# Kernel optimization log

Measured on AMD Instinct MI355X. Metric: run time of the kernel, lower is better.

The kernel has to match this reference:

```python
import jax, jax.numpy as jnp
import numpy as np

HID = 128
HEADS = 4
CH = HID // HEADS          # 32
EDGE_DIM = 2 * HID         # H_update mode
GROUPS = 8
NEG_SLOPE = 0.2
EPS_GN = 1e-5
EPS_LN = 1e-5
N_NODES = 32768
N_EDGES = 524288


def setup_inputs() -> dict:
    key = jax.random.key(0)
    ks = jax.random.split(key, 32)
    N, E, C = N_NODES, N_EDGES, HID
    s = lambda fan: 1.0 / np.sqrt(fan)
    inp = dict(
        h_target=jax.random.normal(ks[0], (N, C), jnp.float32),
        h_source=jax.random.normal(ks[1], (N, C), jnp.float32),
        pos=jax.random.normal(ks[2], (N, 2), jnp.float32),
        t_emb=jax.random.normal(ks[3], (N, C), jnp.float32),
        edge_index=jax.random.randint(ks[4], (2, E), 0, N, jnp.int32),
        # AdaGN params
        gn_gamma=jnp.ones((C,), jnp.float32),
        gn_beta=jnp.zeros((C,), jnp.float32),
        fc_W=jax.random.normal(ks[5], (C, 2 * C), jnp.float32) * s(C),
        fc_b=jnp.zeros((2 * C,), jnp.float32),
        # GATv2 params
        Wl=jax.random.normal(ks[6], (C, HEADS * CH), jnp.float32) * s(C),
        bl=jnp.zeros((HEADS * CH,), jnp.float32),
        Wr=jax.random.normal(ks[7], (C, HEADS * CH), jnp.float32) * s(C),
        br=jnp.zeros((HEADS * CH,), jnp.float32),
        We=jax.random.normal(ks[8], (EDGE_DIM, HEADS * CH), jnp.float32) * s(EDGE_DIM),
        att=jax.random.normal(ks[9], (HEADS, CH), jnp.float32) * s(CH),
        gat_bias=jnp.zeros((HEADS * CH,), jnp.float32),
        # post GAT linear
        Wpost=jax.random.normal(ks[10], (C, C), jnp.float32) * s(C),
        bpost=jnp.zeros((C,), jnp.float32),
        # update MLP: LayerNorm -> Linear -> GELU -> Linear
        ln_g=jnp.ones((C,), jnp.float32),
        ln_b=jnp.zeros((C,), jnp.float32),
        W1=jax.random.normal(ks[11], (C, C), jnp.float32) * s(C),
        b1=jnp.zeros((C,), jnp.float32),
        W2=jax.random.normal(ks[12], (C, C), jnp.float32) * s(C),
        b2=jnp.zeros((C,), jnp.float32),
    )
    return inp


def _adagn(x, cond, gn_gamma, gn_beta, fc_W, fc_b):
    N, C = x.shape
    xg = x.reshape(N, GROUPS, C // GROUPS)
    mu = xg.mean(-1, keepdims=True)
    var = xg.var(-1, keepdims=True)
    normed = ((xg - mu) * jax.lax.rsqrt(var + EPS_GN)).reshape(N, C)
    normed = normed * gn_gamma + gn_beta
    style = cond @ fc_W + fc_b
    gamma, beta = jnp.split(style, 2, axis=-1)
    return normed * (1.0 + gamma) + beta


def reference(h_target, h_source, pos, t_emb, edge_index,
              gn_gamma, gn_beta, fc_W, fc_b,
              Wl, bl, Wr, br, We, att, gat_bias,
              Wpost, bpost, ln_g, ln_b, W1, b1, W2, b2):
    N, C = h_source.shape
    src, dst = edge_index[0], edge_index[1]

    h_src_mod = _adagn(h_source, t_emb, gn_gamma, gn_beta, fc_W, fc_b)

    # physics edge features (H_update mode)
    d_vec = pos[src] - pos[dst]                       # [E,2]
    dx, dy = d_vec[:, 0:1], d_vec[:, 1:2]
    dist_sq = jnp.maximum((d_vec ** 2).sum(-1, keepdims=True), 1e-8)
    grad_mag = (h_src_mod[src] - h_src_mod[dst]) / dist_sq   # [E,C]
    edge_attr = jnp.concatenate([grad_mag * (-dy), grad_mag * dx], axis=-1)  # [E,2C]

    # GATv2Conv (eval mode, no dropout)
    xl = (h_src_mod @ Wl + bl).reshape(N, HEADS, CH)  # source transform
    xr = (h_src_mod @ Wr + br).reshape(N, HEADS, CH)  # target transform
    e = (edge_attr @ We).reshape(-1, HEADS, CH)
    z = jax.nn.leaky_relu(xl[src] + xr[dst] + e, NEG_SLOPE)   # [E,H,Ch]
    logit = jnp.einsum('ehc,hc->eh', z, att)                  # [E,H]
    m = jax.ops.segment_max(logit, dst, num_segments=N)       # [N,H]
    m = jnp.where(jnp.isfinite(m), m, 0.0)
    ex = jnp.exp(logit - m[dst])
    denom = jax.ops.segment_sum(ex, dst, num_segments=N)      # [N,H]
    alpha = ex / (denom[dst] + 1e-16)                         # [E,H]
    msg = xl[src] * alpha[..., None]                          # [E,H,Ch]
    aggr = jax.ops.segment_sum(msg, dst, num_segments=N).reshape(N, HEADS * CH)
    aggr = aggr + gat_bias

    aggr = aggr @ Wpost + bpost

    # update MLP with residual
    mu = aggr.mean(-1, keepdims=True)
    var = aggr.var(-1, keepdims=True)
    ln = (aggr - mu) * jax.lax.rsqrt(var + EPS_LN) * ln_g + ln_b
    h = jax.nn.gelu(ln @ W1 + b1, approximate=False) @ W2 + b2
    return h_target + h
```

## Files before the change

kernel.cpp:

```cpp
#include <hip/hip_runtime.h>
#include <hip/hip_bf16.h>
#include <math.h>

#define HID 128

typedef __bf16 bf16x8 __attribute__((ext_vector_type(8)));
typedef float f32x4 __attribute__((ext_vector_type(4)));
typedef float nf4 __attribute__((ext_vector_type(4)));
union BF8 { uint4 u; bf16x8 v; unsigned short s[8]; };

__device__ __forceinline__ unsigned short f2bf(float x) {
  unsigned u = __float_as_uint(x);
  unsigned r = u + 0x7FFFu + ((u >> 16) & 1u);
  return (unsigned short)(r >> 16);
}
__device__ __forceinline__ float bf2f(unsigned short h) {
  return __uint_as_float(((unsigned)h) << 16);
}
__device__ __forceinline__ void ld2bf(const unsigned short* p, float& x, float& y) {
  unsigned v = *(const unsigned*)p;
  x = __uint_as_float((v & 0xFFFFu) << 16);
  y = __uint_as_float(v & 0xFFFF0000u);
}
__device__ __forceinline__ float2 pk_add2(float2 a, float2 b) {
  return make_float2(a.x + b.x, a.y + b.y);
}
__device__ __forceinline__ float2 pk_sub2(float2 a, float2 b) {
  return make_float2(a.x - b.x, a.y - b.y);
}
__device__ __forceinline__ float2 pk_fma2(float2 a, float2 b, float2 c) {
  return make_float2(fmaf(a.x, b.x, c.x), fmaf(a.y, b.y, c.y));
}
__device__ __forceinline__ float2 pk_max2(float2 a, float2 b) {
  return make_float2(fmaxf(a.x, b.x), fmaxf(a.y, b.y));
}
__device__ __forceinline__ float2 pk_muls2(float2 a, float b) {
  return make_float2(a.x * b, a.y * b);
}

__global__ void prep3(const float* __restrict__ fc_W, const float* __restrict__ Wl,
                      const float* __restrict__ Wr, const float* __restrict__ We,
                      const float* __restrict__ Wpost, const float* __restrict__ W1,
                      const float* __restrict__ W2, const float* __restrict__ bl,
                      const float* __restrict__ br, const float* __restrict__ gat_bias,
                      const float* __restrict__ bpost,
                      unsigned short* __restrict__ fcTh, unsigned short* __restrict__ fcTl,
                      unsigned short* __restrict__ WnTh, unsigned short* __restrict__ WnTl,
                      unsigned short* __restrict__ WpT, unsigned short* __restrict__ W1T,
                      unsigned short* __restrict__ W2T,
                      float* __restrict__ bxy, float* __restrict__ bpost2) {
  int gid = blockIdx.x * 256 + threadIdx.x;
  if (gid < 32768) {
    int n = gid >> 7, k = gid & 127;
    float x = fc_W[k * 256 + n];
    unsigned short h = f2bf(x);
    fcTh[n * 128 + k] = h;
    fcTl[n * 128 + k] = f2bf(x - bf2f(h));
  } else if (gid < 98304) {
    int i = gid - 32768; int n = i >> 7, k = i & 127;
    float x;
    if (n < 128)      x = Wl[k * 128 + n];
    else if (n < 256) x = Wr[k * 128 + (n - 128)];
    else if (n < 384) x = We[k * 128 + (n - 256)];
    else              x = We[(128 + k) * 128 + (n - 384)];
    unsigned short h = f2bf(x);
    WnTh[n * 128 + k] = h;
    if (n >= 256) WnTl[(n - 256) * 128 + k] = f2bf(x - bf2f(h));
  } else if (gid < 147456) {
    int i = gid - 98304; int which = i >> 14; int j = i & 16383;
    int n = j >> 7, k = j & 127;
    const float* W = (which == 0) ? Wpost : (which == 1) ? W1 : W2;
    unsigned short* T = (which == 0) ? WpT : (which == 1) ? W1T : W2T;
    T[n * 128 + k] = f2bf(W[k * 128 + n]);
  } else if (gid < 147712) {
    int j = gid - 147456;
    bxy[j] = (j < 128) ? bl[j] : br[j - 128];
  } else if (gid < 147840) {
    int t = gid - 147712;
    float s = bpost[t];
    for (int k = 0; k < 128; ++k) s += gat_bias[k] * Wpost[k * 128 + t];
    bpost2[t] = s;
  }
}

__global__ __launch_bounds__(256) void gemm_mfma(const float* __restrict__ A,
                                                 const unsigned short* __restrict__ WTh,
                                                 const unsigned short* __restrict__ WTl,
                                                 const float* __restrict__ bias,
                                                 float* __restrict__ C, int Ncols) {
  int tid = threadIdx.x;
  int wave = tid >> 6, lane = tid & 63;
  int m = lane & 15, q = lane >> 4;
  int r0 = blockIdx.x * 64 + wave * 16;
  const float* arow = A + (size_t)(r0 + m) * 128 + q * 8;
  BF8 Ah[4], Al[4];
#pragma unroll
  for (int kc = 0; kc < 4; ++kc) {
    float4 x0 = *(const float4*)(arow + kc * 32);
    float4 x1 = *(const float4*)(arow + kc * 32 + 4);
    float xs[8] = {x0.x, x0.y, x0.z, x0.w, x1.x, x1.y, x1.z, x1.w};
#pragma unroll
    for (int j = 0; j < 8; ++j) {
      unsigned short h = f2bf(xs[j]);
      Ah[kc].s[j] = h;
      Al[kc].s[j] = f2bf(xs[j] - bf2f(h));
    }
  }
  int ntiles = Ncols >> 4;
  for (int nt = 0; nt < ntiles; ++nt) {
    const unsigned short* wr  = WTh + (size_t)(nt * 16 + m) * 128 + q * 8;
    const unsigned short* wrl = WTl + (size_t)(nt * 16 + m) * 128 + q * 8;
    f32x4 acc = {0.f, 0.f, 0.f, 0.f};
#pragma unroll
    for (int kc = 0; kc < 4; ++kc) {
      BF8 bh, blo;
      bh.u  = *(const uint4*)(wr + kc * 32);
      blo.u = *(const uint4*)(wrl + kc * 32);
      acc = __builtin_amdgcn_mfma_f32_16x16x32_bf16(Ah[kc].v, bh.v, acc, 0, 0, 0);
      acc = __builtin_amdgcn_mfma_f32_16x16x32_bf16(Al[kc].v, bh.v, acc, 0, 0, 0);
      acc = __builtin_amdgcn_mfma_f32_16x16x32_bf16(Ah[kc].v, blo.v, acc, 0, 0, 0);
    }
    int n = nt * 16 + m;
    float bv = bias ? bias[n] : 0.0f;
#pragma unroll
    for (int i = 0; i < 4; ++i) {
      int row = r0 + q * 4 + i;
      C[(size_t)row * Ncols + n] = acc[i] + bv;
    }
  }
}

__global__ __launch_bounds__(256) void k_nodeP(const float* __restrict__ h_source,
                                               const float* __restrict__ style,
                                               const float* __restrict__ gn_gamma,
                                               const float* __restrict__ gn_beta,
                                               const unsigned short* __restrict__ WnTh,
                                               const unsigned short* __restrict__ WnTl,
                                               const float* __restrict__ bxy,
                                               unsigned short* __restrict__ packed,
                                               unsigned short* __restrict__ xrArr) {
  int tid = threadIdx.x, wave = tid >> 6, lane = tid & 63;
  int m = lane & 15, q = lane >> 4;
  int r0 = blockIdx.x * 128 + wave * 32;
  BF8 Ah[2][4], Al[2][4];
#pragma unroll
  for (int set = 0; set < 2; ++set) {
    int r = r0 + set * 16 + m;
    const float* hrow = h_source + (size_t)r * 128;
    const float* srow = style + (size_t)r * 256;
#pragma unroll
    for (int kc = 0; kc < 4; ++kc) {
      int ch = q * 8 + kc * 32;
      float4 x0 = *(const float4*)(hrow + ch);
      float4 x1 = *(const float4*)(hrow + ch + 4);
      float xs[8] = {x0.x, x0.y, x0.z, x0.w, x1.x, x1.y, x1.z, x1.w};
      float s8 = 0.f, q8 = 0.f;
#pragma unroll
      for (int j = 0; j < 8; ++j) { s8 += xs[j]; q8 += xs[j] * xs[j]; }
      float s16 = s8 + __shfl_xor(s8, 16);
      float q16 = q8 + __shfl_xor(q8, 16);
      float mu = s16 * (1.0f / 16.0f);
      float var = q16 * (1.0f / 16.0f) - mu * mu;
      float rv = rsqrtf(var + 1e-5f);
      float4 g0 = *(const float4*)(gn_gamma + ch);
      float4 g1 = *(const float4*)(gn_gamma + ch + 4);
      float4 be0 = *(const float4*)(gn_beta + ch);
      float4 be1 = *(const float4*)(gn_beta + ch + 4);
      float4 sg0 = *(const float4*)(srow + ch);
      float4 sg1 = *(const float4*)(srow + ch + 4);
      float4 sb0 = *(const float4*)(srow + 128 + ch);
      float4 sb1 = *(const float4*)(srow + 128 + ch + 4);
      float gg[8] = {g0.x, g0.y, g0.z, g0.w, g1.x, g1.y, g1.z, g1.w};
      float bb[8] = {be0.x, be0.y, be0.z, be0.w, be1.x, be1.y, be1.z, be1.w};
      float sg[8] = {sg0.x, sg0.y, sg0.z, sg0.w, sg1.x, sg1.y, sg1.z, sg1.w};
      float sb[8] = {sb0.x, sb0.y, sb0.z, sb0.w, sb1.x, sb1.y, sb1.z, sb1.w};
#pragma unroll
      for (int j = 0; j < 8; ++j) {
        float v = ((xs[j] - mu) * rv * gg[j] + bb[j]) * (1.0f + sg[j]) + sb[j];
        unsigned short h = f2bf(v);
        Ah[set][kc].s[j] = h;
        Al[set][kc].s[j] = f2bf(v - bf2f(h));
      }
    }
  }
  for (int nt = 0; nt < 32; ++nt) {
    f32x4 acc0 = {0.f, 0.f, 0.f, 0.f};
    f32x4 acc1 = {0.f, 0.f, 0.f, 0.f};
    const unsigned short* wr = WnTh + (size_t)(nt * 16 + m) * 128 + q * 8;
    if (nt < 16) {
#pragma unroll
      for (int kc = 0; kc < 4; ++kc) {
        BF8 bh; bh.u = *(const uint4*)(wr + kc * 32);
        acc0 = __builtin_amdgcn_mfma_f32_16x16x32_bf16(Ah[0][kc].v, bh.v, acc0, 0, 0, 0);
        acc1 = __builtin_amdgcn_mfma_f32_16x16x32_bf16(Ah[1][kc].v, bh.v, acc1, 0, 0, 0);
      }
    } else {
      const unsigned short* wl = WnTl + (size_t)((nt - 16) * 16 + m) * 128 + q * 8;
#pragma unroll
      for (int kc = 0; kc < 4; ++kc) {
        BF8 bh, blo;
        bh.u  = *(const uint4*)(wr + kc * 32);
        blo.u = *(const uint4*)(wl + kc * 32);
        acc0 = __builtin_amdgcn_mfma_f32_16x16x32_bf16(Ah[0][kc].v, bh.v, acc0, 0, 0, 0);
        acc0 = __builtin_amdgcn_mfma_f32_16x16x32_bf16(Al[0][kc].v, bh.v, acc0, 0, 0, 0);
        acc0 = __builtin_amdgcn_mfma_f32_16x16x32_bf16(Ah[0][kc].v, blo.v, acc0, 0, 0, 0);
        acc1 = __builtin_amdgcn_mfma_f32_16x16x32_bf16(Ah[1][kc].v, bh.v, acc1, 0, 0, 0);
        acc1 = __builtin_amdgcn_mfma_f32_16x16x32_bf16(Al[1][kc].v, bh.v, acc1, 0, 0, 0);
        acc1 = __builtin_amdgcn_mfma_f32_16x16x32_bf16(Ah[1][kc].v, blo.v, acc1, 0, 0, 0);
      }
    }
    int n = nt * 16 + m;
    float bv = (nt < 16) ? bxy[n] : 0.0f;
#pragma unroll
    for (int set = 0; set < 2; ++set) {
      f32x4 a = set ? acc1 : acc0;
#pragma unroll
      for (int i = 0; i < 4; ++i) {
        int row = r0 + set * 16 + q * 4 + i;
        unsigned short h = f2bf(a[i] + bv);
        if (nt < 8)       packed[(size_t)row * 384 + n] = h;
        else if (nt < 16) xrArr[(size_t)row * 128 + (n - 128)] = h;
        else              packed[(size_t)row * 384 + 128 + (n - 256)] = h;
      }
    }
  }
}

__global__ __launch_bounds__(256) void k_hist(const int* __restrict__ edst,
                                              int* __restrict__ count, int E) {
  int e = blockIdx.x * 256 + threadIdx.x;
  if (e < E) atomicAdd(&count[edst[e]], 1);
}

__global__ __launch_bounds__(1024) void k_scan(const int* __restrict__ count,
                                               int* __restrict__ rowptr,
                                               int* __restrict__ cursor, int N, int E) {
  __shared__ int wtot[16];
  int t = threadIdx.x;
  int lane = t & 63, wv = t >> 6;
  int base4 = t * 8;
  int4 L[8];
  int s = 0;
#pragma unroll
  for (int i = 0; i < 8; ++i) {
    L[i] = ((const int4*)count)[base4 + i];
    s += L[i].x + L[i].y + L[i].z + L[i].w;
  }
  int incl = s;
#pragma unroll
  for (int off = 1; off < 64; off <<= 1) {
    int v = __shfl_up(incl, off);
    if (lane >= off) incl += v;
  }
  if (lane == 63) wtot[wv] = incl;
  __syncthreads();
  if (t < 16) {
    int v = wtot[t];
    int sc = v;
#pragma unroll
    for (int off = 1; off < 16; off <<= 1) {
      int u = __shfl_up(sc, off, 16);
      if (t >= off) sc += u;
    }
    wtot[t] = sc - v;
  }
  __syncthreads();
  int run = wtot[wv] + (incl - s);
#pragma unroll
  for (int i = 0; i < 8; ++i) {
    int4 c = L[i];
    int4 r;
    r.x = run; run += c.x;
    r.y = run; run += c.y;
    r.z = run; run += c.z;
    r.w = run; run += c.w;
    ((int4*)rowptr)[base4 + i] = r;
    ((int4*)cursor)[base4 + i] = r;
  }
  if (t == 1023) rowptr[N] = E;
}

__global__ __launch_bounds__(256) void k_scatter(const int* __restrict__ esrc,
                                                 const int* __restrict__ edst,
                                                 const float* __restrict__ pos,
                                                 int* __restrict__ cursor,
                                                 nf4* __restrict__ meta, int E) {
  int e = blockIdx.x * 256 + threadIdx.x;
  if (e >= E) return;
  int src = esrc[e], dst = edst[e];
  int p = atomicAdd(&cursor[dst], 1);
  float2 ps = *(const float2*)(pos + 2 * src);
  float2 pd = *(const float2*)(pos + 2 * dst);
  float dx = ps.x - pd.x, dy = ps.y - pd.y;
  float d2 = fmaxf(dx * dx + dy * dy, 1e-8f);
  nf4 v = {__int_as_float(src), -dy / d2, dx / d2, 0.0f};
  __builtin_nontemporal_store(v, &meta[p]);
}

__device__ __forceinline__ void edge_step(nf4 mt, const unsigned* __restrict__ packedW,
                                          int lane, float2 xr, float2 Ad, float2 Bd,
                                          float a0, float a1,
                                          float& m, float& l, float2& s) {
  int si = __float_as_int(mt.x);
  const unsigned* pr = packedW + (size_t)si * 192;
  unsigned wxl = pr[lane];
  unsigned wA  = pr[64 + lane];
  unsigned wB  = pr[128 + lane];
  float2 xl = make_float2(__uint_as_float(wxl << 16), __uint_as_float(wxl & 0xFFFF0000u));
  float2 A  = make_float2(__uint_as_float(wA << 16),  __uint_as_float(wA & 0xFFFF0000u));
  float2 B  = make_float2(__uint_as_float(wB << 16),  __uint_as_float(wB & 0xFFFF0000u));
  float2 z = pk_add2(xl, xr);
  z = pk_fma2(make_float2(mt.y, mt.y), pk_sub2(A, Ad), z);
  z = pk_fma2(make_float2(mt.z, mt.z), pk_sub2(B, Bd), z);
  float2 zl = pk_max2(z, pk_muls2(z, 0.2f));
  float p = fmaf(a0, zl.x, a1 * zl.y);
#pragma unroll
  for (int mm = 8; mm >= 1; mm >>= 1) p += __shfl_xor(p, mm);
  if (p <= m) {
    float ex = expf(p - m);
    l += ex;
    s = pk_fma2(make_float2(ex, ex), xl, s);
  } else {
    float sc = expf(m - p);
    l = fmaf(l, sc, 1.0f);
    s = pk_fma2(make_float2(sc, sc), s, xl);
    m = p;
  }
}

__global__ __launch_bounds__(256) void k_edge(const int* __restrict__ rowptr,
                                              const nf4* __restrict__ meta,
                                              const unsigned short* __restrict__ packed,
                                              const unsigned short* __restrict__ xrArr,
                                              const float* __restrict__ att,
                                              float* __restrict__ aggr, int N) {
  int tid = threadIdx.x;
  int d = blockIdx.x * 4 + (tid >> 6);
  if (d >= N) return;
  int lane = tid & 63;
  int c0 = lane * 2;
  float2 av = *(const float2*)(att + c0);
  const unsigned* packedW = (const unsigned*)packed;
  float2 xr, Ad, Bd;
  ld2bf(xrArr + (size_t)d * 128 + c0, xr.x, xr.y);
  {
    const unsigned* pd = packedW + (size_t)d * 192;
    unsigned wA = pd[64 + lane], wB = pd[128 + lane];
    Ad = make_float2(__uint_as_float(wA << 16), __uint_as_float(wA & 0xFFFF0000u));
    Bd = make_float2(__uint_as_float(wB << 16), __uint_as_float(wB & 0xFFFF0000u));
  }
  int beg = rowptr[d], end = rowptr[d + 1];
  float m1 = -INFINITY, l1 = 0.f; float2 s1 = make_float2(0.f, 0.f);
  float m2 = -INFINITY, l2 = 0.f; float2 s2 = make_float2(0.f, 0.f);
  int j = beg;
  for (; j + 1 < end; j += 2) {
    nf4 mta = __builtin_nontemporal_load(&meta[j]);
    nf4 mtb = __builtin_nontemporal_load(&meta[j + 1]);
    edge_step(mta, packedW, lane, xr, Ad, Bd, av.x, av.y, m1, l1, s1);
    edge_step(mtb, packedW, lane, xr, Ad, Bd, av.x, av.y, m2, l2, s2);
  }
  if (j < end) {
    nf4 mta = __builtin_nontemporal_load(&meta[j]);
    edge_step(mta, packedW, lane, xr, Ad, Bd, av.x, av.y, m1, l1, s1);
  }
  float nm = fmaxf(m1, m2);
  float sc1 = (m1 == nm) ? 1.0f : expf(m1 - nm);
  float sc2 = (m2 == nm) ? 1.0f : expf(m2 - nm);
  float l = fmaf(l1, sc1, l2 * sc2);
  float o0 = fmaf(s1.x, sc1, s2.x * sc2);
  float o1 = fmaf(s1.y, sc1, s2.y * sc2);
  float inv = 1.0f / (l + 1e-16f);
  *(float2*)&aggr[(size_t)d * 128 + c0] = make_float2(o0 * inv, o1 * inv);
}

__global__ __launch_bounds__(256) void k_mlp(const float* __restrict__ aggr,
                                             const unsigned short* __restrict__ WpT,
                                             const unsigned short* __restrict__ W1T,
                                             const unsigned short* __restrict__ W2T,
                                             const float* __restrict__ bpost2,
                                             const float* __restrict__ b1,
                                             const float* __restrict__ b2,
                                             const float* __restrict__ ln_g,
                                             const float* __restrict__ ln_b,
                                             const float* __restrict__ h_target,
                                             float* __restrict__ out) {
  __shared__ unsigned short Tb[64 * 136];
  __shared__ unsigned short Ub[64 * 136];
  int tid = threadIdx.x, wave = tid >> 6, lane = tid & 63;
  int m = lane & 15, q = lane >> 4;
  int r0 = blockIdx.x * 64 + wave * 16;
  int rb0 = wave * 16;
  BF8 Af[4];
  {
    const float* arow = aggr + (size_t)(r0 + m) * 128 + q * 8;
#pragma unroll
    for (int kc = 0; kc < 4; ++kc) {
      float4 x0 = *(const float4*)(arow + kc * 32);
      float4 x1 = *(const float4*)(arow + kc * 32 + 4);
      float xs[8] = {x0.x, x0.y, x0.z, x0.w, x1.x, x1.y, x1.z, x1.w};
#pragma unroll
      for (int jj = 0; jj < 8; ++jj) Af[kc].s[jj] = f2bf(xs[jj]);
    }
  }
  f32x4 acc[8];
#pragma unroll
  for (int t = 0; t < 8; ++t) {
    const unsigned short* wr = WpT + (size_t)(t * 16 + m) * 128 + q * 8;
    f32x4 a = {0.f, 0.f, 0.f, 0.f};
#pragma unroll
    for (int kc = 0; kc < 4; ++kc) {
      BF8 bh; bh.u = *(const uint4*)(wr + kc * 32);
      a = __builtin_amdgcn_mfma_f32_16x16x32_bf16(Af[kc].v, bh.v, a, 0, 0, 0);
    }
    acc[t] = a;
  }
  float sum[4] = {0, 0, 0, 0}, sq[4] = {0, 0, 0, 0};
#pragma unroll
  for (int t = 0; t < 8; ++t) {
    float bv = bpost2[t * 16 + m];
#pragma unroll
    for (int i = 0; i < 4; ++i) {
      float v = acc[t][i] + bv;
      acc[t][i] = v;
      sum[i] += v;
      sq[i] += v * v;
    }
  }
#pragma unroll
  for (int i = 0; i < 4; ++i) {
#pragma unroll
    for (int w = 1; w <= 8; w <<= 1) {
      sum[i] += __shfl_xor(sum[i], w);
      sq[i] += __shfl_xor(sq[i], w);
    }
  }
  float mu[4], rv[4];
#pragma unroll
  for (int i = 0; i < 4; ++i) {
    mu[i] = sum[i] * (1.0f / 128.0f);
    float var = sq[i] * (1.0f / 128.0f) - mu[i] * mu[i];
    rv[i] = rsqrtf(var + 1e-5f);
  }
#pragma unroll
  for (int t = 0; t < 8; ++t) {
    int n = t * 16 + m;
    float g = ln_g[n], b = ln_b[n];
#pragma unroll
    for (int i = 0; i < 4; ++i) {
      float v = (acc[t][i] - mu[i]) * rv[i] * g + b;
      Tb[(rb0 + q * 4 + i) * 136 + n] = f2bf(v);
    }
  }
  __syncthreads();
  BF8 Bf[4];
  {
    const unsigned short* tp = Tb + (rb0 + m) * 136 + q * 8;
#pragma unroll
    for (int kc = 0; kc < 4; ++kc) Bf[kc].u = *(const uint4*)(tp + kc * 32);
  }
#pragma unroll
  for (int t = 0; t < 8; ++t) {
    const unsigned short* wr = W1T + (size_t)(t * 16 + m) * 128 + q * 8;
    f32x4 a = {0.f, 0.f, 0.f, 0.f};
#pragma unroll
    for (int kc = 0; kc < 4; ++kc) {
      BF8 bh; bh.u = *(const uint4*)(wr + kc * 32);
      a = __builtin_amdgcn_mfma_f32_16x16x32_bf16(Bf[kc].v, bh.v, a, 0, 0, 0);
    }
    acc[t] = a;
  }
#pragma unroll
  for (int t = 0; t < 8; ++t) {
    int n = t * 16 + m;
    float bv = b1[n];
#pragma unroll
    for (int i = 0; i < 4; ++i) {
      float v = acc[t][i] + bv;
      v = 0.5f * v * (1.0f + erff(v * 0.70710678118654752f));
      Ub[(rb0 + q * 4 + i) * 136 + n] = f2bf(v);
    }
  }
  __syncthreads();
  BF8 Cf[4];
  {
    const unsigned short* up = Ub + (rb0 + m) * 136 + q * 8;
#pragma unroll
    for (int kc = 0; kc < 4; ++kc) Cf[kc].u = *(const uint4*)(up + kc * 32);
  }
#pragma unroll
  for (int t = 0; t < 8; ++t) {
    const unsigned short* wr = W2T + (size_t)(t * 16 + m) * 128 + q * 8;
    f32x4 a = {0.f, 0.f, 0.f, 0.f};
#pragma unroll
    for (int kc = 0; kc < 4; ++kc) {
      BF8 bh; bh.u = *(const uint4*)(wr + kc * 32);
      a = __builtin_amdgcn_mfma_f32_16x16x32_bf16(Cf[kc].v, bh.v, a, 0, 0, 0);
    }
    int n = t * 16 + m;
    float bv = b2[n];
#pragma unroll
    for (int i = 0; i < 4; ++i) {
      size_t off = (size_t)(r0 + q * 4 + i) * 128 + n;
      out[off] = a[i] + bv + h_target[off];
    }
  }
}

extern "C" void kernel_launch(void* const* d_in, const int* in_sizes, int n_in,
                              void* d_out, int out_size, void* d_ws, size_t ws_size,
                              hipStream_t stream) {
  const float* h_target = (const float*)d_in[0];
  const float* h_source = (const float*)d_in[1];
  const float* pos      = (const float*)d_in[2];
  const float* t_emb    = (const float*)d_in[3];
  const int*   eidx     = (const int*)d_in[4];
  const float* gn_gamma = (const float*)d_in[5];
  const float* gn_beta  = (const float*)d_in[6];
  const float* fc_W     = (const float*)d_in[7];
  const float* fc_b     = (const float*)d_in[8];
  const float* Wl       = (const float*)d_in[9];
  const float* bl       = (const float*)d_in[10];
  const float* Wr       = (const float*)d_in[11];
  const float* br       = (const float*)d_in[12];
  const float* We       = (const float*)d_in[13];
  const float* att      = (const float*)d_in[14];
  const float* gat_bias = (const float*)d_in[15];
  const float* Wpost    = (const float*)d_in[16];
  const float* bpost    = (const float*)d_in[17];
  const float* ln_g     = (const float*)d_in[18];
  const float* ln_b     = (const float*)d_in[19];
  const float* W1       = (const float*)d_in[20];
  const float* b1       = (const float*)d_in[21];
  const float* W2       = (const float*)d_in[22];
  const float* b2       = (const float*)d_in[23];

  const int N = in_sizes[0] / HID;
  const int E = in_sizes[4] / 2;
  const int* esrc = eidx;
  const int* edst = eidx + E;

  float* ws = (float*)d_ws;
  const size_t MF = 1024 * 1024;
  float* style  = ws;
  float* aggr   = ws;
  unsigned short* packed = (unsigned short*)(ws + 8 * MF);
  unsigned short* xrArr  = (unsigned short*)(ws + 14 * MF);
  nf4*   meta   = (nf4*)(ws + 16 * MF);
  int*   rowptr = (int*)(ws + 18 * MF);
  int*   count  = rowptr + 32832;
  int*   cursor = count + 32832;
  unsigned short* wgt = (unsigned short*)(ws + 18 * MF + 131072);
  unsigned short* fcTh = wgt;
  unsigned short* fcTl = wgt + 32768;
  unsigned short* WnTh = wgt + 65536;
  unsigned short* WnTl = wgt + 131072;
  unsigned short* WpT  = wgt + 163840;
  unsigned short* W1T  = wgt + 180224;
  unsigned short* W2T  = wgt + 196608;
  float* bxy    = (float*)(wgt + 212992);
  float* bpost2 = bxy + 256;
  const size_t needed = (size_t)(18 * MF + 131072 + 106496 + 512) * 4;
  if (ws_size < needed) return;

  dim3 blk(256);

  prep3<<<578, blk, 0, stream>>>(fc_W, Wl, Wr, We, Wpost, W1, W2, bl, br, gat_bias, bpost,
                                 fcTh, fcTl, WnTh, WnTl, WpT, W1T, W2T, bxy, bpost2);
  gemm_mfma<<<N / 64, blk, 0, stream>>>(t_emb, fcTh, fcTl, fc_b, style, 256);
  k_nodeP<<<N / 128, blk, 0, stream>>>(h_source, style, gn_gamma, gn_beta, WnTh, WnTl, bxy,
                                       packed, xrArr);
  (void)hipMemsetAsync(count, 0, (size_t)N * 4, stream);
  k_hist<<<(E + 255) / 256, blk, 0, stream>>>(edst, count, E);
  k_scan<<<1, 1024, 0, stream>>>(count, rowptr, cursor, N, E);
  k_scatter<<<(E + 255) / 256, blk, 0, stream>>>(esrc, edst, pos, cursor, meta, E);
  k_edge<<<(N + 3) / 4, blk, 0, stream>>>(rowptr, meta, packed, xrArr, att, aggr, N);
  k_mlp<<<N / 64, blk, 0, stream>>>(aggr, WpT, W1T, W2T, bpost2, b1, b2, ln_g, ln_b,
                                    h_target, (float*)d_out);
}
```

Measured before the change: 394.1 us.

## Fuse CSR build stages into node-side kernels to cut launches

The separate histogram, scan and scatter kernels are folded into the weight-prep, style-GEMM and node-projection kernels as extra block ranges, so independent work shares each launch and the launch count drops from eight to five. The scan is moved into a single 256-thread block inside the style GEMM kernel, where each thread serially sums 32 int4 values. The edge loop now software-prefetches the next pair of meta records and uses normal loads and stores instead of nontemporal ones. The scan block may lengthen the style kernel's tail, and the cache hint changes may alter memory behaviour.

```diff
diff --git a/kernel.cpp b/kernel.cpp
--- a/kernel.cpp
+++ b/kernel.cpp
@@ -38,18 +38,26 @@
   return make_float2(a.x * b, a.y * b);
 }
 
-__global__ void prep3(const float* __restrict__ fc_W, const float* __restrict__ Wl,
-                      const float* __restrict__ Wr, const float* __restrict__ We,
-                      const float* __restrict__ Wpost, const float* __restrict__ W1,
-                      const float* __restrict__ W2, const float* __restrict__ bl,
-                      const float* __restrict__ br, const float* __restrict__ gat_bias,
-                      const float* __restrict__ bpost,
-                      unsigned short* __restrict__ fcTh, unsigned short* __restrict__ fcTl,
-                      unsigned short* __restrict__ WnTh, unsigned short* __restrict__ WnTl,
-                      unsigned short* __restrict__ WpT, unsigned short* __restrict__ W1T,
-                      unsigned short* __restrict__ W2T,
-                      float* __restrict__ bxy, float* __restrict__ bpost2) {
-  int gid = blockIdx.x * 256 + threadIdx.x;
+__global__ __launch_bounds__(256) void k1_prep_hist(
+    const float* __restrict__ fc_W, const float* __restrict__ Wl,
+    const float* __restrict__ Wr, const float* __restrict__ We,
+    const float* __restrict__ Wpost, const float* __restrict__ W1,
+    const float* __restrict__ W2, const float* __restrict__ bl,
+    const float* __restrict__ br, const float* __restrict__ gat_bias,
+    const float* __restrict__ bpost,
+    unsigned short* __restrict__ fcTh, unsigned short* __restrict__ fcTl,
+    unsigned short* __restrict__ WnTh, unsigned short* __restrict__ WnTl,
+    unsigned short* __restrict__ WpT, unsigned short* __restrict__ W1T,
+    unsigned short* __restrict__ W2T,
+    float* __restrict__ bxy, float* __restrict__ bpost2,
+    const int* __restrict__ edst, int* __restrict__ count, int E) {
+  int bid = blockIdx.x;
+  if (bid >= 578) {
+    int e = (bid - 578) * 256 + threadIdx.x;
+    if (e < E) atomicAdd(&count[edst[e]], 1);
+    return;
+  }
+  int gid = bid * 256 + threadIdx.x;
   if (gid < 32768) {
     int n = gid >> 7, k = gid & 127;
     float x = fc_W[k * 256 + n];
@@ -83,11 +91,49 @@
   }
 }
 
-__global__ __launch_bounds__(256) void gemm_mfma(const float* __restrict__ A,
-                                                 const unsigned short* __restrict__ WTh,
-                                                 const unsigned short* __restrict__ WTl,
-                                                 const float* __restrict__ bias,
-                                                 float* __restrict__ C, int Ncols) {
+__global__ __launch_bounds__(256) void k2_style_scan(
+    const float* __restrict__ A, const unsigned short* __restrict__ WTh,
+    const unsigned short* __restrict__ WTl, const float* __restrict__ bias,
+    float* __restrict__ C,
+    const int* __restrict__ count, int* __restrict__ rowptr,
+    int* __restrict__ cursor, int N, int E) {
+  if (blockIdx.x == 512) {
+    __shared__ int wtot[4];
+    int t = threadIdx.x, lane = t & 63, wv = t >> 6;
+    const int4* c4 = (const int4*)count;
+    int base = t * 32;
+    int s = 0;
+    for (int i = 0; i < 32; ++i) {
+      int4 c = c4[base + i];
+      s += c.x + c.y + c.z + c.w;
+    }
+    int incl = s;
+#pragma unroll
+    for (int off = 1; off < 64; off <<= 1) {
+      int v = __shfl_up(incl, off);
+      if (lane >= off) incl += v;
+    }
+    if (lane == 63) wtot[wv] = incl;
+    __syncthreads();
+    if (t == 0) {
+      int a0 = wtot[0], a1 = wtot[1], a2 = wtot[2];
+      wtot[0] = 0; wtot[1] = a0; wtot[2] = a0 + a1; wtot[3] = a0 + a1 + a2;
+    }
+    __syncthreads();
+    int run = wtot[wv] + incl - s;
+    for (int i = 0; i < 32; ++i) {
+      int4 c = c4[base + i];
+      int4 r;
+      r.x = run; run += c.x;
+      r.y = run; run += c.y;
+      r.z = run; run += c.z;
+      r.w = run; run += c.w;
+      ((int4*)rowptr)[base + i] = r;
+      ((int4*)cursor)[base + i] = r;
+    }
+    if (t == 255) rowptr[N] = E;
+    return;
+  }
   int tid = threadIdx.x;
   int wave = tid >> 6, lane = tid & 63;
   int m = lane & 15, q = lane >> 4;
@@ -106,8 +152,7 @@
       Al[kc].s[j] = f2bf(xs[j] - bf2f(h));
     }
   }
-  int ntiles = Ncols >> 4;
-  for (int nt = 0; nt < ntiles; ++nt) {
+  for (int nt = 0; nt < 16; ++nt) {
     const unsigned short* wr  = WTh + (size_t)(nt * 16 + m) * 128 + q * 8;
     const unsigned short* wrl = WTl + (size_t)(nt * 16 + m) * 128 + q * 8;
     f32x4 acc = {0.f, 0.f, 0.f, 0.f};
@@ -121,27 +166,41 @@
       acc = __builtin_amdgcn_mfma_f32_16x16x32_bf16(Ah[kc].v, blo.v, acc, 0, 0, 0);
     }
     int n = nt * 16 + m;
-    float bv = bias ? bias[n] : 0.0f;
+    float bv = bias[n];
 #pragma unroll
     for (int i = 0; i < 4; ++i) {
       int row = r0 + q * 4 + i;
-      C[(size_t)row * Ncols + n] = acc[i] + bv;
-    }
-  }
-}
-
-__global__ __launch_bounds__(256) void k_nodeP(const float* __restrict__ h_source,
-                                               const float* __restrict__ style,
-                                               const float* __restrict__ gn_gamma,
-                                               const float* __restrict__ gn_beta,
-                                               const unsigned short* __restrict__ WnTh,
-                                               const unsigned short* __restrict__ WnTl,
-                                               const float* __restrict__ bxy,
-                                               unsigned short* __restrict__ packed,
-                                               unsigned short* __restrict__ xrArr) {
+      C[(size_t)row * 256 + n] = acc[i] + bv;
+    }
+  }
+}
+
+__global__ __launch_bounds__(256) void k3_node_scatter(
+    const float* __restrict__ h_source, const float* __restrict__ style,
+    const float* __restrict__ gn_gamma, const float* __restrict__ gn_beta,
+    const unsigned short* __restrict__ WnTh, const unsigned short* __restrict__ WnTl,
+    const float* __restrict__ bxy,
+    unsigned short* __restrict__ packed, unsigned short* __restrict__ xrArr,
+    const int* __restrict__ esrc, const int* __restrict__ edst,
+    const float* __restrict__ pos, int* __restrict__ cursor,
+    nf4* __restrict__ meta, int E) {
+  int bid = blockIdx.x;
+  if (bid >= 256) {
+    int e = (bid - 256) * 256 + threadIdx.x;
+    if (e >= E) return;
+    int src = esrc[e], dst = edst[e];
+    int p = atomicAdd(&cursor[dst], 1);
+    float2 ps = *(const float2*)(pos + 2 * src);
+    float2 pd = *(const float2*)(pos + 2 * dst);
+    float dx = ps.x - pd.x, dy = ps.y - pd.y;
+    float d2 = fmaxf(dx * dx + dy * dy, 1e-8f);
+    nf4 v = {__int_as_float(src), -dy / d2, dx / d2, 0.0f};
+    meta[p] = v;
+    return;
+  }
   int tid = threadIdx.x, wave = tid >> 6, lane = tid & 63;
   int m = lane & 15, q = lane >> 4;
-  int r0 = blockIdx.x * 128 + wave * 32;
+  int r0 = bid * 128 + wave * 32;
   BF8 Ah[2][4], Al[2][4];
 #pragma unroll
   for (int set = 0; set < 2; ++set) {
@@ -224,77 +283,6 @@
       }
     }
   }
-}
-
-__global__ __launch_bounds__(256) void k_hist(const int* __restrict__ edst,
-                                              int* __restrict__ count, int E) {
-  int e = blockIdx.x * 256 + threadIdx.x;
-  if (e < E) atomicAdd(&count[edst[e]], 1);
-}
-
-__global__ __launch_bounds__(1024) void k_scan(const int* __restrict__ count,
-                                               int* __restrict__ rowptr,
-                                               int* __restrict__ cursor, int N, int E) {
-  __shared__ int wtot[16];
-  int t = threadIdx.x;
-  int lane = t & 63, wv = t >> 6;
-  int base4 = t * 8;
-  int4 L[8];
-  int s = 0;
-#pragma unroll
-  for (int i = 0; i < 8; ++i) {
-    L[i] = ((const int4*)count)[base4 + i];
-    s += L[i].x + L[i].y + L[i].z + L[i].w;
-  }
-  int incl = s;
-#pragma unroll
-  for (int off = 1; off < 64; off <<= 1) {
-    int v = __shfl_up(incl, off);
-    if (lane >= off) incl += v;
-  }
-  if (lane == 63) wtot[wv] = incl;
-  __syncthreads();
-  if (t < 16) {
-    int v = wtot[t];
-    int sc = v;
-#pragma unroll
-    for (int off = 1; off < 16; off <<= 1) {
-      int u = __shfl_up(sc, off, 16);
-      if (t >= off) sc += u;
-    }
-    wtot[t] = sc - v;
-  }
-  __syncthreads();
-  int run = wtot[wv] + (incl - s);
-#pragma unroll
-  for (int i = 0; i < 8; ++i) {
-    int4 c = L[i];
-    int4 r;
-    r.x = run; run += c.x;
-    r.y = run; run += c.y;
-    r.z = run; run += c.z;
-    r.w = run; run += c.w;
-    ((int4*)rowptr)[base4 + i] = r;
-    ((int4*)cursor)[base4 + i] = r;
-  }
-  if (t == 1023) rowptr[N] = E;
-}
-
-__global__ __launch_bounds__(256) void k_scatter(const int* __restrict__ esrc,
-                                                 const int* __restrict__ edst,
-                                                 const float* __restrict__ pos,
-                                                 int* __restrict__ cursor,
-                                                 nf4* __restrict__ meta, int E) {
-  int e = blockIdx.x * 256 + threadIdx.x;
-  if (e >= E) return;
-  int src = esrc[e], dst = edst[e];
-  int p = atomicAdd(&cursor[dst], 1);
-  float2 ps = *(const float2*)(pos + 2 * src);
-  float2 pd = *(const float2*)(pos + 2 * dst);
-  float dx = ps.x - pd.x, dy = ps.y - pd.y;
-  float d2 = fmaxf(dx * dx + dy * dy, 1e-8f);
-  nf4 v = {__int_as_float(src), -dy / d2, dx / d2, 0.0f};
-  __builtin_nontemporal_store(v, &meta[p]);
 }
 
 __device__ __forceinline__ void edge_step(nf4 mt, const unsigned* __restrict__ packedW,
@@ -353,15 +341,21 @@
   float m1 = -INFINITY, l1 = 0.f; float2 s1 = make_float2(0.f, 0.f);
   float m2 = -INFINITY, l2 = 0.f; float2 s2 = make_float2(0.f, 0.f);
   int j = beg;
-  for (; j + 1 < end; j += 2) {
-    nf4 mta = __builtin_nontemporal_load(&meta[j]);
-    nf4 mtb = __builtin_nontemporal_load(&meta[j + 1]);
-    edge_step(mta, packedW, lane, xr, Ad, Bd, av.x, av.y, m1, l1, s1);
-    edge_step(mtb, packedW, lane, xr, Ad, Bd, av.x, av.y, m2, l2, s2);
+  if (j + 1 < end) {
+    nf4 mt0 = meta[j], mt1 = meta[j + 1];
+    for (; j + 3 < end; j += 2) {
+      nf4 nx0 = meta[j + 2], nx1 = meta[j + 3];
+      edge_step(mt0, packedW, lane, xr, Ad, Bd, av.x, av.y, m1, l1, s1);
+      edge_step(mt1, packedW, lane, xr, Ad, Bd, av.x, av.y, m2, l2, s2);
+      mt0 = nx0; mt1 = nx1;
+    }
+    edge_step(mt0, packedW, lane, xr, Ad, Bd, av.x, av.y, m1, l1, s1);
+    edge_step(mt1, packedW, lane, xr, Ad, Bd, av.x, av.y, m2, l2, s2);
+    j += 2;
   }
   if (j < end) {
-    nf4 mta = __builtin_nontemporal_load(&meta[j]);
-    edge_step(mta, packedW, lane, xr, Ad, Bd, av.x, av.y, m1, l1, s1);
+    nf4 mt = meta[j];
+    edge_step(mt, packedW, lane, xr, Ad, Bd, av.x, av.y, m1, l1, s1);
   }
   float nm = fmaxf(m1, m2);
   float sc1 = (m1 == nm) ? 1.0f : expf(m1 - nm);
@@ -563,16 +557,17 @@
   if (ws_size < needed) return;
 
   dim3 blk(256);
-
-  prep3<<<578, blk, 0, stream>>>(fc_W, Wl, Wr, We, Wpost, W1, W2, bl, br, gat_bias, bpost,
-                                 fcTh, fcTl, WnTh, WnTl, WpT, W1T, W2T, bxy, bpost2);
-  gemm_mfma<<<N / 64, blk, 0, stream>>>(t_emb, fcTh, fcTl, fc_b, style, 256);
-  k_nodeP<<<N / 128, blk, 0, stream>>>(h_source, style, gn_gamma, gn_beta, WnTh, WnTl, bxy,
-                                       packed, xrArr);
+  const int histB = (E + 255) / 256;
+
   (void)hipMemsetAsync(count, 0, (size_t)N * 4, stream);
-  k_hist<<<(E + 255) / 256, blk, 0, stream>>>(edst, count, E);
-  k_scan<<<1, 1024, 0, stream>>>(count, rowptr, cursor, N, E);
-  k_scatter<<<(E + 255) / 256, blk, 0, stream>>>(esrc, edst, pos, cursor, meta, E);
+  k1_prep_hist<<<578 + histB, blk, 0, stream>>>(
+      fc_W, Wl, Wr, We, Wpost, W1, W2, bl, br, gat_bias, bpost,
+      fcTh, fcTl, WnTh, WnTl, WpT, W1T, W2T, bxy, bpost2, edst, count, E);
+  k2_style_scan<<<513, blk, 0, stream>>>(t_emb, fcTh, fcTl, fc_b, style,
+                                         count, rowptr, cursor, N, E);
+  k3_node_scatter<<<256 + histB, blk, 0, stream>>>(
+      h_source, style, gn_gamma, gn_beta, WnTh, WnTl, bxy, packed, xrArr,
+      esrc, edst, pos, cursor, meta, E);
   k_edge<<<(N + 3) / 4, blk, 0, stream>>>(rowptr, meta, packed, xrArr, att, aggr, N);
   k_mlp<<<N / 64, blk, 0, stream>>>(aggr, WpT, W1T, W2T, bpost2, b1, b2, ln_g, ln_b,
                                     h_target, (float*)d_out);
```

After: 363.5 us. -7.7%, faster.
